# Performance work log

Measured on AMD Instinct MI355X. Metric: run time of the kernel, lower is better.

Reference implementation:

```python
import jax, jax.numpy as jnp
import numpy as np

K = 3
PAD = 1
STRIDE = 1


def _unfold(x, k, pad, stride):
    """torch.nn.Unfold equivalent: [B,C,H,W] -> [B, C*k*k, L], feature order (c, ki, kj)."""
    B, C, H, W = x.shape
    xp = jnp.pad(x, ((0, 0), (0, 0), (pad, pad), (pad, pad)))
    Ho = (H + 2 * pad - k) // stride + 1
    Wo = (W + 2 * pad - k) // stride + 1
    # k*k strided views stacked on a new patch axis -> [B, C, k*k, Ho, Wo]
    cols = jnp.stack(
        [xp[:, :, i : i + (Ho - 1) * stride + 1 : stride,
                 j : j + (Wo - 1) * stride + 1 : stride]
         for i in range(k) for j in range(k)],
        axis=2,
    )
    return cols.reshape(B, C * k * k, Ho * Wo)


def setup_inputs() -> dict:
    key = jax.random.key(0)
    k1, k2 = jax.random.split(key)
    B, C, H, W = 4, 64, 128, 128
    return {
        "key_map": jax.random.normal(k1, (B, C, H, W), dtype=jnp.float32),
        "query_map": jax.random.normal(k2, (B, C, H, W), dtype=jnp.float32),
    }


def reference(key_map, query_map):
    B, C = key_map.shape[0], key_map.shape[1]
    kk = K * K
    # torch .view of [B, C*k^2, L] to [B, C, L, k^2] is a raw row-major
    # reinterpretation; jnp.reshape reproduces it exactly.
    ku = _unfold(key_map, K, PAD, STRIDE).reshape(B, C, -1, kk)
    qu = _unfold(query_map, K, PAD, STRIDE).reshape(B, C, -1, kk)
    c = kk // 2  # center-patch slice index
    out1 = ku * qu[:, :, :, c : c + 1]
    out2 = ku[:, :, :, c : c + 1] * qu
    return (out1, out2)
```

## Files before the change

kernel.cpp:

```cpp
#include <hip/hip_runtime.h>


#define LPP   16384
#define NPP   147456
#define HW    128

__device__ __forceinline__ int unfold_off(int n, bool& valid) {
    const int p  = n >> 14;
    const int l  = n & (LPP - 1);
    const int ho = l >> 7;
    const int wo = l & (HW - 1);
    const int ki = p / 3;
    const int kj = p - 3 * ki;
    const int h  = ho + ki - 1;
    const int w  = wo + kj - 1;
    valid = ((unsigned)h < (unsigned)HW) && ((unsigned)w < (unsigned)HW);
    return h * HW + w;
}

extern "C" __global__ __launch_bounds__(256) void depen_kernel(
    const float* __restrict__ key, const float* __restrict__ qry,
    float* __restrict__ out1, float* __restrict__ out2)
{
    const int bc = blockIdx.y;
    const int n0 = 4 * (blockIdx.x * 256 + threadIdx.x);

    const float* __restrict__ kp = key + (size_t)bc * LPP;
    const float* __restrict__ qp = qry + (size_t)bc * LPP;

    const int p   = n0 >> 14;
    const int l0  = n0 & (LPP - 1);
    const int ho  = l0 >> 7;
    const int wo0 = l0 & (HW - 1);
    const int ki  = p / 3;
    const int kj  = p - 3 * ki;
    const int h   = ho + ki - 1;

    float kv[4], qv[4];
    if ((unsigned)h < (unsigned)HW) {
        const int base = h * HW + wo0 + kj - 1;
        kv[1] = kp[base + 1];  qv[1] = qp[base + 1];
        kv[2] = kp[base + 2];  qv[2] = qp[base + 2];
        const bool v0 = (wo0 + kj) > 0;
        const bool v3 = (wo0 + kj + 2) < HW;
        kv[0] = v0 ? kp[base]     : 0.0f;
        qv[0] = v0 ? qp[base]     : 0.0f;
        kv[3] = v3 ? kp[base + 3] : 0.0f;
        qv[3] = v3 ? qp[base + 3] : 0.0f;
    } else {
        kv[0]=kv[1]=kv[2]=kv[3]=0.0f;
        qv[0]=qv[1]=qv[2]=qv[3]=0.0f;
    }

    const int i0 = n0 / 9;
    const int r  = n0 - 9 * i0;
    const int i1 = (n0 + 3) / 9;

    bool va, vb;
    const int offa = unfold_off(9 * i0 + 4, va);
    const int offb = unfold_off(9 * i1 + 4, vb);
    const float ck0 = va ? kp[offa] : 0.0f;
    const float cq0 = va ? qp[offa] : 0.0f;
    const float ck1 = vb ? kp[offb] : 0.0f;
    const float cq1 = vb ? qp[offb] : 0.0f;

    float o1[4], o2[4];
    #pragma unroll
    for (int e = 0; e < 4; ++e) {
        const bool first = (r + e) < 9;
        const float cq = first ? cq0 : cq1;
        const float ck = first ? ck0 : ck1;
        o1[e] = kv[e] * cq;
        o2[e] = ck * qv[e];
    }

    const size_t ob = (size_t)bc * NPP + n0;
    *reinterpret_cast<float4*>(out1 + ob) = make_float4(o1[0], o1[1], o1[2], o1[3]);
    *reinterpret_cast<float4*>(out2 + ob) = make_float4(o2[0], o2[1], o2[2], o2[3]);
}

extern "C" void kernel_launch(void* const* d_in, const int* in_sizes, int n_in,
                              void* d_out, int out_size, void* d_ws, size_t ws_size,
                              hipStream_t stream) {
    const float* key = (const float*)d_in[0];
    const float* qry = (const float*)d_in[1];
    float* out1 = (float*)d_out;
    float* out2 = out1 + (size_t)256 * NPP;

    dim3 grid(144, 256, 1);
    dim3 block(256, 1, 1);
    depen_kernel<<<grid, block, 0, stream>>>(key, qry, out1, out2);
}
```

Before: 376.2 us.

## Process eight outputs per thread with nontemporal stores and XCD-aware block remap

Each thread now produces eight consecutive outputs instead of four, halving the thread count and amortising index math and the centre-value loads. Output stores use nontemporal builtins so the large write-only stream does not pollute the cache. The 2D grid becomes a flat grid whose block index is remapped so consecutive slices are grouped by XCD (b&7), with the aim of improving L2 locality for the shared input reads. This raises register use per thread and depends on the remap being a correct bijection over 18432 blocks.

```diff
diff --git a/kernel.cpp b/kernel.cpp
--- a/kernel.cpp
+++ b/kernel.cpp
@@ -4,6 +4,8 @@
 #define LPP   16384
 #define NPP   147456
 #define HW    128
+
+typedef float v4f __attribute__((ext_vector_type(4)));
 
 __device__ __forceinline__ int unfold_off(int n, bool& valid) {
     const int p  = n >> 14;
@@ -22,8 +24,12 @@
     const float* __restrict__ key, const float* __restrict__ qry,
     float* __restrict__ out1, float* __restrict__ out2)
 {
-    const int bc = blockIdx.y;
-    const int n0 = 4 * (blockIdx.x * 256 + threadIdx.x);
+    const int b  = blockIdx.x;
+    const int u  = (b & 7) * 2304 + (b >> 3);
+    const int bc = u / 72;
+    const int xb = u - 72 * bc;
+
+    const int n0 = 8 * (xb * 256 + (int)threadIdx.x);
 
     const float* __restrict__ kp = key + (size_t)bc * LPP;
     const float* __restrict__ qp = qry + (size_t)bc * LPP;
@@ -36,25 +42,28 @@
     const int kj  = p - 3 * ki;
     const int h   = ho + ki - 1;
 
-    float kv[4], qv[4];
+    float kv[8], qv[8];
     if ((unsigned)h < (unsigned)HW) {
         const int base = h * HW + wo0 + kj - 1;
-        kv[1] = kp[base + 1];  qv[1] = qp[base + 1];
-        kv[2] = kp[base + 2];  qv[2] = qp[base + 2];
+        #pragma unroll
+        for (int e = 1; e <= 6; ++e) {
+            kv[e] = kp[base + e];
+            qv[e] = qp[base + e];
+        }
         const bool v0 = (wo0 + kj) > 0;
-        const bool v3 = (wo0 + kj + 2) < HW;
+        const bool v7 = (wo0 + kj) < 122;
         kv[0] = v0 ? kp[base]     : 0.0f;
         qv[0] = v0 ? qp[base]     : 0.0f;
-        kv[3] = v3 ? kp[base + 3] : 0.0f;
-        qv[3] = v3 ? qp[base + 3] : 0.0f;
+        kv[7] = v7 ? kp[base + 7] : 0.0f;
+        qv[7] = v7 ? qp[base + 7] : 0.0f;
     } else {
-        kv[0]=kv[1]=kv[2]=kv[3]=0.0f;
-        qv[0]=qv[1]=qv[2]=qv[3]=0.0f;
+        #pragma unroll
+        for (int e = 0; e < 8; ++e) { kv[e] = 0.0f; qv[e] = 0.0f; }
     }
 
     const int i0 = n0 / 9;
     const int r  = n0 - 9 * i0;
-    const int i1 = (n0 + 3) / 9;
+    const int i1 = (n0 + 7) / 9;
 
     bool va, vb;
     const int offa = unfold_off(9 * i0 + 4, va);
@@ -64,19 +73,27 @@
     const float ck1 = vb ? kp[offb] : 0.0f;
     const float cq1 = vb ? qp[offb] : 0.0f;
 
-    float o1[4], o2[4];
+    const size_t ob = (size_t)bc * NPP + n0;
+
+    float o[8];
     #pragma unroll
-    for (int e = 0; e < 4; ++e) {
-        const bool first = (r + e) < 9;
-        const float cq = first ? cq0 : cq1;
-        const float ck = first ? ck0 : ck1;
-        o1[e] = kv[e] * cq;
-        o2[e] = ck * qv[e];
+    for (int e = 0; e < 8; ++e)
+        o[e] = kv[e] * (((r + e) < 9) ? cq0 : cq1);
+    {
+        v4f w0; w0.x=o[0]; w0.y=o[1]; w0.z=o[2]; w0.w=o[3];
+        v4f w1; w1.x=o[4]; w1.y=o[5]; w1.z=o[6]; w1.w=o[7];
+        __builtin_nontemporal_store(w0, reinterpret_cast<v4f*>(out1 + ob));
+        __builtin_nontemporal_store(w1, reinterpret_cast<v4f*>(out1 + ob + 4));
     }
-
-    const size_t ob = (size_t)bc * NPP + n0;
-    *reinterpret_cast<float4*>(out1 + ob) = make_float4(o1[0], o1[1], o1[2], o1[3]);
-    *reinterpret_cast<float4*>(out2 + ob) = make_float4(o2[0], o2[1], o2[2], o2[3]);
+    #pragma unroll
+    for (int e = 0; e < 8; ++e)
+        o[e] = (((r + e) < 9) ? ck0 : ck1) * qv[e];
+    {
+        v4f w0; w0.x=o[0]; w0.y=o[1]; w0.z=o[2]; w0.w=o[3];
+        v4f w1; w1.x=o[4]; w1.y=o[5]; w1.z=o[6]; w1.w=o[7];
+        __builtin_nontemporal_store(w0, reinterpret_cast<v4f*>(out2 + ob));
+        __builtin_nontemporal_store(w1, reinterpret_cast<v4f*>(out2 + ob + 4));
+    }
 }
 
 extern "C" void kernel_launch(void* const* d_in, const int* in_sizes, int n_in,
@@ -87,7 +104,7 @@
     float* out1 = (float*)d_out;
     float* out2 = out1 + (size_t)256 * NPP;
 
-    dim3 grid(144, 256, 1);
+    dim3 grid(18432, 1, 1);
     dim3 block(256, 1, 1);
     depen_kernel<<<grid, block, 0, stream>>>(key, qry, out1, out2);
 }
```

Result: faster. 357.6 us (-5.0%).
